# Kernel optimization log

Measured on AMD Instinct MI355X. Metric: run time of the kernel, lower is better.

The kernel has to match this reference:

```python
import jax, jax.numpy as jnp
import numpy as np

L, B, E, H, HID = 2048, 4, 512, 8, 2048
HD = E // H


def setup_inputs() -> dict:
    key = jax.random.key(0)
    ks = jax.random.split(key, 6)
    s = 0.02
    x = jax.random.normal(ks[0], (L, B, E), jnp.float32)
    in_proj_w = jax.random.normal(ks[1], (3 * E, E), jnp.float32) * s
    in_proj_b = jnp.zeros((3 * E,), jnp.float32)
    out_w = jax.random.normal(ks[2], (E, E), jnp.float32) * s
    out_b = jnp.zeros((E,), jnp.float32)
    w1 = jax.random.normal(ks[3], (HID, E), jnp.float32) * s  # torch Linear: (out, in)
    b1 = jnp.zeros((HID,), jnp.float32)
    w2 = jax.random.normal(ks[4], (E, HID), jnp.float32) * s
    b2 = jnp.zeros((E,), jnp.float32)
    ln_g = jnp.ones((E,), jnp.float32)
    ln_b = jnp.zeros((E,), jnp.float32)
    return {"x": x, "in_proj_w": in_proj_w, "in_proj_b": in_proj_b,
            "out_w": out_w, "out_b": out_b, "w1": w1, "b1": b1,
            "w2": w2, "b2": b2, "ln_g": ln_g, "ln_b": ln_b}


def _pos_encoding(S, Emb, dtype):
    # even i: sin((t+1) * 10000^(-i/E)); odd i: cos((t+1) * 10000^(-(i+1)/E))
    t = jnp.arange(S, dtype=dtype)[:, None]
    i = jnp.arange(Emb, dtype=dtype)[None, :]
    even = jnp.sin((t + 1.0) * jnp.power(10000.0, -i / Emb))
    odd = jnp.cos((t + 1.0) * jnp.power(10000.0, -(i + 1.0) / Emb))
    return jnp.where(jnp.arange(Emb)[None, :] % 2 == 0, even, odd)  # (S, Emb)


def _layernorm(x, g, b, eps=1e-5):
    mu = jnp.mean(x, axis=-1, keepdims=True)
    var = jnp.mean(jnp.square(x - mu), axis=-1, keepdims=True)
    return (x - mu) * jax.lax.rsqrt(var + eps) * g + b


def _mha(x, in_proj_w, in_proj_b, out_w, out_b):
    # x: (L, B, E); self-attention, torch MultiheadAttention semantics
    qkv = jnp.einsum('lbe,fe->lbf', x, in_proj_w) + in_proj_b
    q, k, v = jnp.split(qkv, 3, axis=-1)
    q = q.reshape(L, B, H, HD)
    k = k.reshape(L, B, H, HD)
    v = v.reshape(L, B, H, HD)
    scores = jnp.einsum('lbhd,mbhd->bhlm', q, k) / np.sqrt(HD).astype(np.float32)
    attn = jax.nn.softmax(scores, axis=-1)
    o = jnp.einsum('bhlm,mbhd->lbhd', attn, v).reshape(L, B, E)
    return jnp.einsum('lbe,fe->lbf', o, out_w) + out_b


def reference(x, in_proj_w, in_proj_b, out_w, out_b, w1, b1, w2, b2, ln_g, ln_b):
    # positional encoding: varies along dim1, broadcasts along dim0 (as in source)
    pe = _pos_encoding(x.shape[1], x.shape[2], x.dtype)  # (B, E)
    x = x + pe[None, :, :]
    # Post-Norm path
    x = _layernorm(_mha(x, in_proj_w, in_proj_b, out_w, out_b) + x, ln_g, ln_b)
    h = jax.nn.gelu(jnp.einsum('lbe,he->lbh', x, w1) + b1, approximate=False)
    ff = jnp.einsum('lbh,eh->lbe', h, w2) + b2
    x = _layernorm(ff + x, ln_g, ln_b)
    return x
```

## Files before the change

### kernel.cpp

```cpp
#include <hip/hip_runtime.h>

typedef unsigned short u16;
typedef unsigned int   u32;
typedef u16  u16x2 __attribute__((ext_vector_type(2)));
typedef u16  u16x4 __attribute__((ext_vector_type(4)));
typedef u16  u16x8 __attribute__((ext_vector_type(8)));
typedef short s8v  __attribute__((ext_vector_type(8)));
typedef short s4v  __attribute__((ext_vector_type(4)));
typedef float f4v  __attribute__((ext_vector_type(4)));
typedef u32  u32x2 __attribute__((ext_vector_type(2)));

#define L_SEQ 2048
#define B_SZ  4
#define E_DIM 512
#define H_CNT 8
#define HD    64
#define HID   2048
#define M_ROWS (L_SEQ * B_SZ)
#define QSCALE 0.18033688011112042f

__device__ __forceinline__ u16 f2b(float f) {
    unsigned u = __builtin_bit_cast(unsigned, f);
    u += 0x7fffu + ((u >> 16) & 1u);
    return (u16)(u >> 16);
}
__device__ __forceinline__ float b2f(u16 u) {
    u32 x = ((u32)u) << 16; return __builtin_bit_cast(float, x);
}
#if defined(__has_builtin)
#if __has_builtin(__builtin_amdgcn_cvt_pk_bf16_f32)
#define HAVE_PK_BF16 1
#endif
#endif
__device__ __forceinline__ u32 pk_trunc(float a, float b) {
#ifdef HAVE_PK_BF16
    typedef __bf16 bf2 __attribute__((ext_vector_type(2)));
    bf2 r = __builtin_amdgcn_cvt_pk_bf16_f32(a, b);
    return __builtin_bit_cast(u32, r);
#else
    u32 ua = __builtin_bit_cast(u32, a), ub = __builtin_bit_cast(u32, b);
    return (ua >> 16) | (ub & 0xffff0000u);
#endif
}
__device__ __forceinline__ void gload_lds16(const u16* g, u16* l) {
    __builtin_amdgcn_global_load_lds((__attribute__((address_space(1))) void*)(u16*)g,
                                     (__attribute__((address_space(3))) void*)l, 16, 0, 0);
}
__device__ __forceinline__ float gelu_f(float v) {
    float y2 = v * (1.5957691216f + 0.0713548576f * v * v);
    return v / (1.0f + __expf(-y2));
}

__global__ __launch_bounds__(256) void pe_tab_k(float* __restrict__ pet) {
    int i = blockIdx.x * 256 + threadIdx.x;
    int e = i & (E_DIM - 1);
    float t = (float)(i >> 9) + 1.0f;
    int ee = (e & 1) ? (e + 1) : e;
    float w = exp2f((-(float)ee / 512.0f) * 13.287712379549449f);
    pet[i] = (e & 1) ? cosf(t * w) : sinf(t * w);
}

__global__ __launch_bounds__(256) void pe_add_k(const float* __restrict__ x,
                                                const float* __restrict__ pet,
                                                u16* __restrict__ xpb) {
    int idx = (blockIdx.x * 256 + threadIdx.x) * 4;
    f4v v = *(const f4v*)(x + idx);
    f4v p = *(const f4v*)(pet + (idx & 2047));
    u16x4 o;
#pragma unroll
    for (int i = 0; i < 4; ++i) o[i] = f2b(v[i] + p[i]);
    *(u16x4*)(xpb + idx) = o;
}

__global__ __launch_bounds__(256) void conv4_k(const float* __restrict__ s1, u16* __restrict__ d1, int n1,
                                               const float* __restrict__ s2, u16* __restrict__ d2, int n2,
                                               const float* __restrict__ s3, u16* __restrict__ d3, int n3,
                                               const float* __restrict__ s4, u16* __restrict__ d4) {
    int o = (blockIdx.x * 256 + threadIdx.x) * 4;
    const float* s; u16* d;
    if (o < n1) { s = s1; d = d1; }
    else { o -= n1;
        if (o < n2) { s = s2; d = d2; }
        else { o -= n2;
            if (o < n3) { s = s3; d = d3; }
            else { o -= n3; s = s4; d = d4; } } }
    f4v v = *(const f4v*)(s + o);
    u16x4 q;
#pragma unroll
    for (int i = 0; i < 4; ++i) q[i] = f2b(v[i]);
    *(u16x4*)(d + o) = q;
}

template <int NP, bool WRITEF, bool WRITEB>
__global__ __launch_bounds__(256)
void ln_c(const u16* __restrict__ p0, const u16* __restrict__ p1,
          const u16* __restrict__ p2, const u16* __restrict__ p3,
          const float* __restrict__ bias, const u16* __restrict__ resid,
          const float* __restrict__ gw, const float* __restrict__ bw,
          float* __restrict__ outF, u16* __restrict__ outB) {
    int wave = threadIdx.x >> 6, lane = threadIdx.x & 63;
    size_t row = (size_t)blockIdx.x * 4 + wave;
    size_t off = row * E_DIM + lane * 8;
    u16x8 rv = *(const u16x8*)(resid + off);
    f4v a, b;
#pragma unroll
    for (int i = 0; i < 4; ++i) { a[i] = b2f(rv[i]); b[i] = b2f(rv[i + 4]); }
    a += *(const f4v*)(bias + lane * 8);
    b += *(const f4v*)(bias + lane * 8 + 4);
    const u16* ps[4] = {p0, p1, p2, p3};
#pragma unroll
    for (int z = 0; z < NP; ++z) {
        u16x8 t = *(const u16x8*)(ps[z] + off);
#pragma unroll
        for (int i = 0; i < 4; ++i) { a[i] += b2f(t[i]); b[i] += b2f(t[i + 4]); }
    }
    float s = (a[0] + a[1]) + (a[2] + a[3]) + (b[0] + b[1]) + (b[2] + b[3]);
#pragma unroll
    for (int o = 1; o < 64; o <<= 1) s += __shfl_xor(s, o, 64);
    float mu = s * (1.0f / E_DIM);
    float q = 0.f;
#pragma unroll
    for (int i = 0; i < 4; ++i) { float d = a[i] - mu; q += d * d; }
#pragma unroll
    for (int i = 0; i < 4; ++i) { float d = b[i] - mu; q += d * d; }
#pragma unroll
    for (int o = 1; o < 64; o <<= 1) q += __shfl_xor(q, o, 64);
    float rstd = rsqrtf(q * (1.0f / E_DIM) + 1e-5f);
    f4v g0 = *(const f4v*)(gw + lane * 8), g1 = *(const f4v*)(gw + lane * 8 + 4);
    f4v w0 = *(const f4v*)(bw + lane * 8), w1 = *(const f4v*)(bw + lane * 8 + 4);
    f4v y0, y1;
#pragma unroll
    for (int i = 0; i < 4; ++i) { y0[i] = (a[i] - mu) * rstd * g0[i] + w0[i];
                                  y1[i] = (b[i] - mu) * rstd * g1[i] + w1[i]; }
    if (WRITEF) {
        *(f4v*)(outF + off)     = y0;
        *(f4v*)(outF + off + 4) = y1;
    }
    if (WRITEB) {
        u16x8 o;
#pragma unroll
        for (int i = 0; i < 4; ++i) { o[i] = f2b(y0[i]); o[i + 4] = f2b(y1[i]); }
        *(u16x8*)(outB + off) = o;
    }
}

__global__ __launch_bounds__(256) void transpose_v_k(const u16* __restrict__ vb,
                                                     u16* __restrict__ vt) {
    __shared__ __align__(16) u16 T[64 * 66];
    int t = threadIdx.x;
    int lt = blockIdx.x, bh = blockIdx.y;
    const u16* src = vb + (size_t)bh * (L_SEQ * HD) + (size_t)lt * 64 * HD;
    int lr = t >> 2, d0 = (t & 3) * 16;
    s8v va = *(const s8v*)(src + lr * HD + d0);
    s8v vb8 = *(const s8v*)(src + lr * HD + d0 + 8);
#pragma unroll
    for (int c = 0; c < 4; ++c) {
        u16x2 p0; p0[0] = (u16)va[c * 2]; p0[1] = (u16)va[c * 2 + 1];
        u16x2 p1; p1[0] = (u16)vb8[c * 2]; p1[1] = (u16)vb8[c * 2 + 1];
        *(u16x2*)(&T[lr * 66 + d0 + c * 2])     = p0;
        *(u16x2*)(&T[lr * 66 + d0 + 8 + c * 2]) = p1;
    }
    __syncthreads();
    int d = t >> 2, l0 = (t & 3) * 16;
    u16 tmp[16];
#pragma unroll
    for (int i = 0; i < 16; ++i) tmp[i] = T[(l0 + i) * 66 + d];
    u16* dst = vt + (size_t)bh * (L_SEQ * HD) + (size_t)d * L_SEQ + lt * 64 + l0;
    u16x8 o0, o1;
#pragma unroll
    for (int i = 0; i < 8; ++i) { o0[i] = tmp[i]; o1[i] = tmp[8 + i]; }
    *(u16x8*)dst       = o0;
    *(u16x8*)(dst + 8) = o1;
}

template <int MODE>
__global__ __launch_bounds__(256, 3)
void gemm_bt(const u16* __restrict__ A, const u16* __restrict__ Bw,
             const float* __restrict__ bias, int M, int N, int K,
             u16* __restrict__ outB,
             u16* __restrict__ oq, u16* __restrict__ okk, u16* __restrict__ ov) {
    __shared__ __align__(16) u16 As[2][128 * 32];
    __shared__ __align__(16) u16 Bs[2][128 * 32];
    const int tid = threadIdx.x;
    const int wave = tid >> 6, lane = tid & 63;
    const int col = lane & 15, quad = lane >> 4;
    const int bm = blockIdx.y * 128, bn = blockIdx.x * 128;
    const int wm = (wave >> 1) * 64, wn = (wave & 1) * 64;
    f4v acc[4][4] = {};
    const int srow = wave * 16 + (lane >> 2);
    const int soff = (lane & 3) * 8;
    const u16* Ag = A + (size_t)(bm + srow) * K + soff;
    const u16* Bg = Bw + (size_t)(bn + srow) * K + soff;
    const int wo = wave * 512;
    for (int kc = 0; kc < K; kc += 64) {
        __syncthreads();
#pragma unroll
        for (int hs = 0; hs < 2; ++hs) {
            gload_lds16(Ag + kc + hs * 32,                  &As[hs][wo]);
            gload_lds16(Ag + (size_t)64 * K + kc + hs * 32, &As[hs][wo + 2048]);
            gload_lds16(Bg + kc + hs * 32,                  &Bs[hs][wo]);
            gload_lds16(Bg + (size_t)64 * K + kc + hs * 32, &Bs[hs][wo + 2048]);
        }
        __syncthreads();
#pragma unroll
        for (int hs = 0; hs < 2; ++hs) {
            s8v af[4], bf[4];
#pragma unroll
            for (int i = 0; i < 4; ++i) af[i] = *(const s8v*)(&As[hs][(wm + i * 16 + col) * 32 + quad * 8]);
#pragma unroll
            for (int j = 0; j < 4; ++j) bf[j] = *(const s8v*)(&Bs[hs][(wn + j * 16 + col) * 32 + quad * 8]);
#pragma unroll
            for (int i = 0; i < 4; ++i)
#pragma unroll
                for (int j = 0; j < 4; ++j)
                    acc[i][j] = __builtin_amdgcn_mfma_f32_16x16x32_bf16(af[i], bf[j], acc[i][j], 0, 0, 0);
        }
    }
#pragma unroll
    for (int j = 0; j < 4; ++j) {
        int gn = bn + wn + j * 16 + col;
        float bv = bias[gn];
        int which = gn >> 9, hh = (gn >> 6) & 7, d = gn & 63;
        u16* dst = (MODE == 0) ? ((which == 0) ? oq : ((which == 1) ? okk : ov)) : outB;
        float qs = (MODE == 0 && which == 0) ? QSCALE : 1.0f;
#pragma unroll
        for (int i = 0; i < 4; ++i) {
            int gm0 = bm + wm + i * 16 + quad * 4;
#pragma unroll
            for (int r = 0; r < 4; ++r) {
                float v = acc[i][j][r] + bv;
                int m = gm0 + r;
                if (MODE == 2) {
                    outB[(size_t)m * N + gn] = f2b(gelu_f(v));
                } else {
                    int l = m >> 2, bb = m & 3;
                    dst[((size_t)(bb * H_CNT + hh) * L_SEQ + l) * HD + d] = f2b(v * qs);
                }
            }
        }
    }
}

__global__ __launch_bounds__(256, 3)
void gemm_ks(const u16* __restrict__ A, const u16* __restrict__ Bw,
             int N, int K, int Kper,
             u16* __restrict__ q0, u16* __restrict__ q1,
             u16* __restrict__ q2, u16* __restrict__ q3) {
    __shared__ __align__(16) u16 As[2][128 * 32];
    __shared__ __align__(16) u16 Bs[2][128 * 32];
    const int tid = threadIdx.x;
    const int wave = tid >> 6, lane = tid & 63;
    const int col = lane & 15, quad = lane >> 4;
    const int bm = blockIdx.y * 128, bn = blockIdx.x * 128;
    const int kz = blockIdx.z;
    u16* pz = (kz == 0) ? q0 : (kz == 1) ? q1 : (kz == 2) ? q2 : q3;
    const int wm = (wave >> 1) * 64, wn = (wave & 1) * 64;
    f4v acc[4][4] = {};
    const int srow = wave * 16 + (lane >> 2);
    const int soff = (lane & 3) * 8;
    const u16* Ag = A + (size_t)(bm + srow) * K + kz * Kper + soff;
    const u16* Bg = Bw + (size_t)(bn + srow) * K + kz * Kper + soff;
    const int wo = wave * 512;
    for (int kc = 0; kc < Kper; kc += 64) {
        __syncthreads();
#pragma unroll
        for (int hs = 0; hs < 2; ++hs) {
            gload_lds16(Ag + kc + hs * 32,                  &As[hs][wo]);
            gload_lds16(Ag + (size_t)64 * K + kc + hs * 32, &As[hs][wo + 2048]);
            gload_lds16(Bg + kc + hs * 32,                  &Bs[hs][wo]);
            gload_lds16(Bg + (size_t)64 * K + kc + hs * 32, &Bs[hs][wo + 2048]);
        }
        __syncthreads();
#pragma unroll
        for (int hs = 0; hs < 2; ++hs) {
            s8v af[4], bf[4];
#pragma unroll
            for (int i = 0; i < 4; ++i) af[i] = *(const s8v*)(&As[hs][(wm + i * 16 + col) * 32 + quad * 8]);
#pragma unroll
            for (int j = 0; j < 4; ++j) bf[j] = *(const s8v*)(&Bs[hs][(wn + j * 16 + col) * 32 + quad * 8]);
#pragma unroll
            for (int i = 0; i < 4; ++i)
#pragma unroll
                for (int j = 0; j < 4; ++j)
                    acc[i][j] = __builtin_amdgcn_mfma_f32_16x16x32_bf16(af[i], bf[j], acc[i][j], 0, 0, 0);
        }
    }
#pragma unroll
    for (int j = 0; j < 4; ++j) {
        int gn = bn + wn + j * 16 + col;
#pragma unroll
        for (int i = 0; i < 4; ++i) {
            int m0 = bm + wm + i * 16 + quad * 4;
#pragma unroll
            for (int r = 0; r < 4; ++r)
                pz[(size_t)(m0 + r) * N + gn] = f2b(acc[i][j][r]);
        }
    }
}

__global__ __launch_bounds__(256, 4)
void attn_k(const u16* __restrict__ qg, const u16* __restrict__ kg,
            const u16* __restrict__ vtg,
            u16* __restrict__ po0, u16* __restrict__ po1,
            u16* __restrict__ po2, u16* __restrict__ po3, float* __restrict__ lbuf) {
    __shared__ __align__(16) u16 Ks[2][2][64 * 32];
    __shared__ __align__(16) u16 Vs[2][2][64 * 32];
    const int tid = threadIdx.x;
    const int wave = tid >> 6, lane = tid & 63;
    const int col = lane & 15, quad = lane >> 4;
    const int qc = blockIdx.x, kz = blockIdx.y, bh = blockIdx.z;
    const size_t base = (size_t)bh * (L_SEQ * HD);
    s8v qf[2][2];
#pragma unroll
    for (int t = 0; t < 2; ++t) {
        const int qrow = qc * 128 + wave * 32 + t * 16 + col;
#pragma unroll
        for (int hh = 0; hh < 2; ++hh)
            qf[t][hh] = *(const s8v*)(qg + base + (size_t)qrow * HD + hh * 32 + quad * 8);
    }
    f4v oa[2][4] = {};
    f4v la[2] = {};
    const s4v vones = {0x3F80, 0x3F80, 0x3F80, 0x3F80};
    const int h = wave & 1, r0 = (wave >> 1) * 16;
    const int srow = lane >> 2, c = lane & 3;
    const int cp = c ^ ((srow >> 1) & 3);
    const u16* Kg = kg + base + (size_t)(r0 + srow) * HD + h * 32 + cp * 8;
    const u16* Vg = vtg + base + (size_t)(r0 + srow) * L_SEQ + h * 32 + cp * 8;
    const int kt0 = kz * 8;
    {
        const int kv0 = kt0 * 64;
        gload_lds16(Kg + (size_t)kv0 * HD,        &Ks[0][h][r0 * 32]);
        gload_lds16(Kg + (size_t)(kv0 + 32) * HD, &Ks[0][h][(r0 + 32) * 32]);
        gload_lds16(Vg + kv0,                     &Vs[0][h][r0 * 32]);
        gload_lds16(Vg + kv0 + (size_t)32 * L_SEQ,&Vs[0][h][(r0 + 32) * 32]);
    }
    const int perm = (col >> 1) & 3;
    for (int it = 0; it < 8; ++it) {
        const int cur = it & 1, nxt = cur ^ 1;
        __syncthreads();
        if (it + 1 < 8) {
            const int kv0 = (kt0 + it + 1) * 64;
            gload_lds16(Kg + (size_t)kv0 * HD,        &Ks[nxt][h][r0 * 32]);
            gload_lds16(Kg + (size_t)(kv0 + 32) * HD, &Ks[nxt][h][(r0 + 32) * 32]);
            gload_lds16(Vg + kv0,                     &Vs[nxt][h][r0 * 32]);
            gload_lds16(Vg + kv0 + (size_t)32 * L_SEQ,&Vs[nxt][h][(r0 + 32) * 32]);
        }
        f4v st[2][4];
#pragma unroll
        for (int j = 0; j < 4; ++j) {
            s8v k0 = *(const s8v*)(&Ks[cur][0][(j * 16 + col) * 32 + ((quad ^ perm) * 8)]);
            s8v k1 = *(const s8v*)(&Ks[cur][1][(j * 16 + col) * 32 + ((quad ^ perm) * 8)]);
#pragma unroll
            for (int t = 0; t < 2; ++t) {
                f4v z = {};
                z = __builtin_amdgcn_mfma_f32_16x16x32_bf16(k0, qf[t][0], z, 0, 0, 0);
                z = __builtin_amdgcn_mfma_f32_16x16x32_bf16(k1, qf[t][1], z, 0, 0, 0);
                st[t][j] = z;
            }
        }
        s4v pt[2][4];
#pragma unroll
        for (int t = 0; t < 2; ++t)
#pragma unroll
            for (int j = 0; j < 4; ++j) {
                f4v p;
#pragma unroll
                for (int r = 0; r < 4; ++r) p[r] = exp2f(st[t][j][r]);
                u32x2 pk;
                pk[0] = pk_trunc(p[0], p[1]);
                pk[1] = pk_trunc(p[2], p[3]);
                pt[t][j] = __builtin_bit_cast(s4v, pk);
            }
#pragma unroll
        for (int cc = 0; cc < 4; ++cc) {
            const int hh = cc >> 1;
            const int ch8 = (cc & 1) * 2 + (quad >> 1);
#pragma unroll
            for (int dj = 0; dj < 4; ++dj) {
                s4v vf = *(const s4v*)(&Vs[cur][hh][(dj * 16 + col) * 32 + ((ch8 ^ perm) * 8) + (quad & 1) * 4]);
#pragma unroll
                for (int t = 0; t < 2; ++t)
                    oa[t][dj] = __builtin_amdgcn_mfma_f32_16x16x16bf16_1k(pt[t][cc], vf, oa[t][dj], 0, 0, 0);
            }
#pragma unroll
            for (int t = 0; t < 2; ++t)
                la[t] = __builtin_amdgcn_mfma_f32_16x16x16bf16_1k(pt[t][cc], vones, la[t], 0, 0, 0);
        }
    }
    if (col == 0) {
#pragma unroll
        for (int t = 0; t < 2; ++t)
#pragma unroll
            for (int r = 0; r < 4; ++r)
                lbuf[kz * 65536 + bh * 2048 + (qc * 128 + wave * 32 + t * 16 + quad * 4 + r)] = la[t][r];
    }
    u16* pg = (kz == 0) ? po0 : (kz == 1) ? po1 : (kz == 2) ? po2 : po3;
    const int b = bh >> 3, hd = bh & 7;
#pragma unroll
    for (int t = 0; t < 2; ++t)
#pragma unroll
        for (int r = 0; r < 4; ++r) {
            int lrow = qc * 128 + wave * 32 + t * 16 + quad * 4 + r;
            size_t mrow = (size_t)(lrow * 4 + b) * E_DIM + hd * HD;
#pragma unroll
            for (int dj = 0; dj < 4; ++dj)
                pg[mrow + dj * 16 + col] = f2b(oa[t][dj][r]);
        }
}

__global__ __launch_bounds__(256)
void combine_k(const u16* __restrict__ p0, const u16* __restrict__ p1,
               const u16* __restrict__ p2, const u16* __restrict__ p3,
               const float* __restrict__ lbuf, u16* __restrict__ out) {
    int idx8 = blockIdx.x * 256 + threadIdx.x;
    int m = idx8 >> 6;
    int e0 = (idx8 & 63) * 8;
    int b = m & 3, lrow = m >> 2, h = e0 >> 6;
    int li = (b * 8 + h) * 2048 + lrow;
    float inv = 1.0f / (lbuf[li] + lbuf[65536 + li] + lbuf[131072 + li] + lbuf[196608 + li]);
    size_t off = (size_t)m * E_DIM + e0;
    u16x8 a0 = *(const u16x8*)(p0 + off);
    u16x8 a1 = *(const u16x8*)(p1 + off);
    u16x8 a2 = *(const u16x8*)(p2 + off);
    u16x8 a3 = *(const u16x8*)(p3 + off);
    u16x8 o;
#pragma unroll
    for (int i = 0; i < 8; ++i)
        o[i] = f2b(((b2f(a0[i]) + b2f(a1[i])) + (b2f(a2[i]) + b2f(a3[i]))) * inv);
    *(u16x8*)(out + off) = o;
}

extern "C" void kernel_launch(void* const* d_in, const int* in_sizes, int n_in,
                              void* d_out, int out_size, void* d_ws, size_t ws_size,
                              hipStream_t stream) {
    const float* x     = (const float*)d_in[0];
    const float* w_qkv = (const float*)d_in[1];
    const float* b_qkv = (const float*)d_in[2];
    const float* w_out = (const float*)d_in[3];
    const float* b_out = (const float*)d_in[4];
    const float* w1    = (const float*)d_in[5];
    const float* b1    = (const float*)d_in[6];
    const float* w2    = (const float*)d_in[7];
    const float* b2    = (const float*)d_in[8];
    const float* ln_g  = (const float*)d_in[9];
    const float* ln_b  = (const float*)d_in[10];

    char* ws = (char*)d_ws;
    u16*   WQKV = (u16*)(ws + 0);
    u16*   WOUT = (u16*)(ws + 1572864);
    u16*   W1B  = (u16*)(ws + 2097152);
    u16*   W2B  = (u16*)(ws + 4194304);
    u16*   XPB  = (u16*)(ws + 6291456);
    u16*   QB   = (u16*)(ws + 14680064);
    u16*   KB   = (u16*)(ws + 23068672);
    u16*   VB   = (u16*)(ws + 31457280);
    u16*   VT   = (u16*)(ws + 39845888);
    u16*   AP0  = (u16*)(ws + 48234496);
    u16*   AP1  = (u16*)(ws + 56623104);
    u16*   AP2  = (u16*)(ws + 65011712);
    u16*   AP3  = (u16*)(ws + 73400320);
    float* LB   = (float*)(ws + 81788928);
    float* PET  = (float*)(ws + 82837504);
    u16*   OB   = VB;
    u16*   OP0  = (u16*)(ws + 48234496);
    u16*   OP1  = (u16*)(ws + 56623104);
    u16*   X3B  = QB;
    u16*   HB   = (u16*)(ws + 48234496);
    u16*   FP0  = XPB;
    u16*   FP1  = KB;

    pe_tab_k<<<8, 256, 0, stream>>>(PET);
    pe_add_k<<<4096, 256, 0, stream>>>(x, PET, XPB);
    conv4_k<<<3072, 256, 0, stream>>>(w_qkv, WQKV, 3 * E_DIM * E_DIM,
                                      w_out, WOUT, E_DIM * E_DIM,
                                      w1, W1B, HID * E_DIM,
                                      w2, W2B);
    gemm_bt<0><<<dim3(12, 64), 256, 0, stream>>>(XPB, WQKV, b_qkv, M_ROWS, 3 * E_DIM, E_DIM,
                                                 nullptr, QB, KB, VB);
    transpose_v_k<<<dim3(32, 32), 256, 0, stream>>>(VB, VT);
    attn_k<<<dim3(16, 4, 32), 256, 0, stream>>>(QB, KB, VT, AP0, AP1, AP2, AP3, LB);
    combine_k<<<2048, 256, 0, stream>>>(AP0, AP1, AP2, AP3, LB, OB);
    gemm_ks<<<dim3(4, 64, 2), 256, 0, stream>>>(OB, WOUT, E_DIM, E_DIM, 256,
                                                OP0, OP1, nullptr, nullptr);
    ln_c<2, false, true><<<2048, 256, 0, stream>>>(OP0, OP1, nullptr, nullptr,
                                                   b_out, XPB, ln_g, ln_b, nullptr, X3B);
    gemm_bt<2><<<dim3(16, 64), 256, 0, stream>>>(X3B, W1B, b1, M_ROWS, HID, E_DIM,
                                                 HB, nullptr, nullptr, nullptr);
    gemm_ks<<<dim3(4, 64, 2), 256, 0, stream>>>(HB, W2B, E_DIM, HID, 1024,
                                                FP0, FP1, nullptr, nullptr);
    ln_c<2, true, false><<<2048, 256, 0, stream>>>(FP0, FP1, nullptr, nullptr,
                                                   b2, X3B, ln_g, ln_b, (float*)d_out, nullptr);
}
```

Baseline: 274.9 us.

## Double-buffer GEMM K-loop to prefetch next slice during MFMA compute

```diff
diff --git a/kernel.cpp b/kernel.cpp
--- a/kernel.cpp
+++ b/kernel.cpp
@@ -174,7 +174,7 @@
 }
 
 template <int MODE>
-__global__ __launch_bounds__(256, 3)
+__global__ __launch_bounds__(256, 4)
 void gemm_bt(const u16* __restrict__ A, const u16* __restrict__ Bw,
              const float* __restrict__ bias, int M, int N, int K,
              u16* __restrict__ outB,
@@ -192,29 +192,31 @@
     const u16* Ag = A + (size_t)(bm + srow) * K + soff;
     const u16* Bg = Bw + (size_t)(bn + srow) * K + soff;
     const int wo = wave * 512;
-    for (int kc = 0; kc < K; kc += 64) {
+    gload_lds16(Ag,                  &As[0][wo]);
+    gload_lds16(Ag + (size_t)64 * K, &As[0][wo + 2048]);
+    gload_lds16(Bg,                  &Bs[0][wo]);
+    gload_lds16(Bg + (size_t)64 * K, &Bs[0][wo + 2048]);
+    const int nit = K >> 5;
+    for (int t = 0; t < nit; ++t) {
+        const int cur = t & 1, nxt = cur ^ 1;
         __syncthreads();
-#pragma unroll
-        for (int hs = 0; hs < 2; ++hs) {
-            gload_lds16(Ag + kc + hs * 32,                  &As[hs][wo]);
-            gload_lds16(Ag + (size_t)64 * K + kc + hs * 32, &As[hs][wo + 2048]);
-            gload_lds16(Bg + kc + hs * 32,                  &Bs[hs][wo]);
-            gload_lds16(Bg + (size_t)64 * K + kc + hs * 32, &Bs[hs][wo + 2048]);
-        }
-        __syncthreads();
-#pragma unroll
-        for (int hs = 0; hs < 2; ++hs) {
-            s8v af[4], bf[4];
-#pragma unroll
-            for (int i = 0; i < 4; ++i) af[i] = *(const s8v*)(&As[hs][(wm + i * 16 + col) * 32 + quad * 8]);
-#pragma unroll
-            for (int j = 0; j < 4; ++j) bf[j] = *(const s8v*)(&Bs[hs][(wn + j * 16 + col) * 32 + quad * 8]);
-#pragma unroll
-            for (int i = 0; i < 4; ++i)
-#pragma unroll
-                for (int j = 0; j < 4; ++j)
-                    acc[i][j] = __builtin_amdgcn_mfma_f32_16x16x32_bf16(af[i], bf[j], acc[i][j], 0, 0, 0);
-        }
+        if (t + 1 < nit) {
+            const int kc = (t + 1) * 32;
+            gload_lds16(Ag + kc,                  &As[nxt][wo]);
+            gload_lds16(Ag + (size_t)64 * K + kc, &As[nxt][wo + 2048]);
+            gload_lds16(Bg + kc,                  &Bs[nxt][wo]);
+            gload_lds16(Bg + (size_t)64 * K + kc, &Bs[nxt][wo + 2048]);
+        }
+        s8v af[4], bf[4];
+#pragma unroll
+        for (int i = 0; i < 4; ++i) af[i] = *(const s8v*)(&As[cur][(wm + i * 16 + col) * 32 + quad * 8]);
+#pragma unroll
+        for (int j = 0; j < 4; ++j) bf[j] = *(const s8v*)(&Bs[cur][(wn + j * 16 + col) * 32 + quad * 8]);
+#pragma unroll
+        for (int i = 0; i < 4; ++i)
+#pragma unroll
+            for (int j = 0; j < 4; ++j)
+                acc[i][j] = __builtin_amdgcn_mfma_f32_16x16x32_bf16(af[i], bf[j], acc[i][j], 0, 0, 0);
     }
 #pragma unroll
     for (int j = 0; j < 4; ++j) {
@@ -241,7 +243,7 @@
     }
 }
 
-__global__ __launch_bounds__(256, 3)
+__global__ __launch_bounds__(256, 4)
 void gemm_ks(const u16* __restrict__ A, const u16* __restrict__ Bw,
              int N, int K, int Kper,
              u16* __restrict__ q0, u16* __restrict__ q1,
@@ -261,29 +263,31 @@
     const u16* Ag = A + (size_t)(bm + srow) * K + kz * Kper + soff;
     const u16* Bg = Bw + (size_t)(bn + srow) * K + kz * Kper + soff;
     const int wo = wave * 512;
-    for (int kc = 0; kc < Kper; kc += 64) {
+    gload_lds16(Ag,                  &As[0][wo]);
+    gload_lds16(Ag + (size_t)64 * K, &As[0][wo + 2048]);
+    gload_lds16(Bg,                  &Bs[0][wo]);
+    gload_lds16(Bg + (size_t)64 * K, &Bs[0][wo + 2048]);
+    const int nit = Kper >> 5;
+    for (int t = 0; t < nit; ++t) {
+        const int cur = t & 1, nxt = cur ^ 1;
         __syncthreads();
-#pragma unroll
-        for (int hs = 0; hs < 2; ++hs) {
-            gload_lds16(Ag + kc + hs * 32,                  &As[hs][wo]);
-            gload_lds16(Ag + (size_t)64 * K + kc + hs * 32, &As[hs][wo + 2048]);
-            gload_lds16(Bg + kc + hs * 32,                  &Bs[hs][wo]);
-            gload_lds16(Bg + (size_t)64 * K + kc + hs * 32, &Bs[hs][wo + 2048]);
-        }
-        __syncthreads();
-#pragma unroll
-        for (int hs = 0; hs < 2; ++hs) {
-            s8v af[4], bf[4];
-#pragma unroll
-            for (int i = 0; i < 4; ++i) af[i] = *(const s8v*)(&As[hs][(wm + i * 16 + col) * 32 + quad * 8]);
-#pragma unroll
-            for (int j = 0; j < 4; ++j) bf[j] = *(const s8v*)(&Bs[hs][(wn + j * 16 + col) * 32 + quad * 8]);
-#pragma unroll
-            for (int i = 0; i < 4; ++i)
-#pragma unroll
-                for (int j = 0; j < 4; ++j)
-                    acc[i][j] = __builtin_amdgcn_mfma_f32_16x16x32_bf16(af[i], bf[j], acc[i][j], 0, 0, 0);
-        }
+        if (t + 1 < nit) {
+            const int kc = (t + 1) * 32;
+            gload_lds16(Ag + kc,                  &As[nxt][wo]);
+            gload_lds16(Ag + (size_t)64 * K + kc, &As[nxt][wo + 2048]);
+            gload_lds16(Bg + kc,                  &Bs[nxt][wo]);
+            gload_lds16(Bg + (size_t)64 * K + kc, &Bs[nxt][wo + 2048]);
+        }
+        s8v af[4], bf[4];
+#pragma unroll
+        for (int i = 0; i < 4; ++i) af[i] = *(const s8v*)(&As[cur][(wm + i * 16 + col) * 32 + quad * 8]);
+#pragma unroll
+        for (int j = 0; j < 4; ++j) bf[j] = *(const s8v*)(&Bs[cur][(wn + j * 16 + col) * 32 + quad * 8]);
+#pragma unroll
+        for (int i = 0; i < 4; ++i)
+#pragma unroll
+            for (int j = 0; j < 4; ++j)
+                acc[i][j] = __builtin_amdgcn_mfma_f32_16x16x32_bf16(af[i], bf[j], acc[i][j], 0, 0, 0);
     }
 #pragma unroll
     for (int j = 0; j < 4; ++j) {
```

Result: no change. 274.4 us (-0.2%).
